# Kernel tuning notes

Hardware: AMD Instinct MI355X
Metric: run time of the kernel (lower is better)

The kernel has to match this reference:

```python
import jax, jax.numpy as jnp
import numpy as np

B, N = 32, 512
NB_TAU, NB_G, NB_W = 8, 8, 6
FLOOR = 0.001
SLOPE_RANGE = (0.5, 4.0)
BIAS_RANGE = (-2.0, 2.0)


def _basis(x, nb, kind):
    # MonotoneBasis: fixed grid of slopes/biases, monotone activation per basis.
    slopes = jnp.asarray(np.linspace(SLOPE_RANGE[0], SLOPE_RANGE[1], nb), x.dtype)
    biases = jnp.asarray(np.linspace(BIAS_RANGE[0], BIAS_RANGE[1], nb), x.dtype)
    z = x[..., None] * slopes + biases  # [..., nb]
    return jax.nn.softplus(z) if kind == 'softplus' else jax.nn.sigmoid(z)


def _normalize_scores(scores, mask, eps=1e-6):
    scores = jnp.where(mask, scores, 0.0)
    denom = jnp.clip(mask.sum(axis=1, keepdims=True), 1)
    mean = scores.sum(axis=1, keepdims=True) / denom
    scores = scores - mean
    var = (scores ** 2 * mask).sum(axis=1, keepdims=True) / denom
    return scores / jnp.sqrt(var + eps)


def setup_inputs() -> dict:
    key = jax.random.key(0)
    k1, k2, k3, k4, k5 = jax.random.split(key, 5)
    return {
        'predictions': jax.random.normal(k1, (B, N), dtype=jnp.float32),
        # targets in [0,1): all valid (no -1 padding), ties have measure zero
        'targets': jax.random.uniform(k2, (B, N), dtype=jnp.float32),
        'theta_tau': jax.random.normal(k3, (NB_TAU,), dtype=jnp.float32) * 0.1,
        'theta_g': jax.random.normal(k4, (NB_G,), dtype=jnp.float32) * 0.1,
        'theta_w': jax.random.normal(k5, (NB_W,), dtype=jnp.float32) * 0.1,
    }


def reference(predictions, targets, theta_tau, theta_g, theta_w):
    mask = ~jnp.isclose(targets, -1.0)
    s = _normalize_scores(predictions, mask)
    r = targets
    n = predictions.shape[1]
    iu, ju = np.triu_indices(n, k=1)  # static pair enumeration, P = n*(n-1)/2

    dr = r[:, iu] - r[:, ju]                      # [B, P]
    t = jnp.sign(dr)
    keep = (t != 0) & mask[:, iu] & mask[:, ju]   # drop ties / padded pairs
    ds = s[:, iu] - s[:, ju]
    abs_dr = jnp.abs(dr)

    # learned nonnegative combination coefficients (monotone outputs)
    c_tau = jax.nn.softplus(theta_tau)
    c_g = jax.nn.softplus(theta_g)
    c_w = jax.nn.softplus(theta_w)

    tau = _basis(abs_dr, NB_TAU, 'softplus') @ c_tau   # learned margin
    m = tau - t * ds
    g = _basis(m, NB_G, 'softplus') @ c_g              # learned penalty
    w = FLOOR + _basis(abs_dr, NB_W, 'sigmoid') @ c_w  # learned gap weight
    pair_loss = g * w

    kf = keep.astype(pair_loss.dtype)
    denom = jnp.clip(kf.sum(axis=1), 1.0)
    row_loss = (pair_loss * kf).sum(axis=1) / denom    # per-row mean over kept pairs
    valid_row = (kf.sum(axis=1) > 0).astype(pair_loss.dtype)
    return (row_loss * valid_row).sum() / jnp.clip(valid_row.sum(), 1.0)
```

## Files before the change

kernel.cpp:

```cpp
#include <hip/hip_runtime.h>
#include <math.h>

#define BB 32
#define NN 512

#define OFF_RS2 0
#define OFF_CF  32768
#define OFF_SUM 32808
#define OFF_CNT 32840

__device__ __forceinline__ float splus(float z) {
    return fmaxf(z, 0.0f) + __logf(1.0f + __expf(-fabsf(z)));
}

__device__ __constant__ float ST8[8] = {0.5f, 1.0f, 1.5f, 2.0f, 2.5f, 3.0f, 3.5f, 4.0f};
__device__ __constant__ float BT8[8] = {
    (float)(-2.0), (float)(-2.0 + 4.0/7.0), (float)(-2.0 + 8.0/7.0),
    (float)(-2.0 + 12.0/7.0), (float)(-2.0 + 16.0/7.0),
    (float)(-2.0 + 20.0/7.0), (float)(-2.0 + 24.0/7.0), 2.0f };
__device__ __constant__ float SW6[6] = {0.5f, (float)(0.5 + 3.5/5.0), (float)(0.5 + 7.0/5.0),
    (float)(0.5 + 10.5/5.0), (float)(0.5 + 14.0/5.0), 4.0f};
__device__ __constant__ float BW6[6] = {-2.0f, (float)(-2.0 + 4.0/5.0), (float)(-2.0 + 8.0/5.0),
    (float)(-2.0 + 12.0/5.0), (float)(-2.0 + 16.0/5.0), 2.0f};

__device__ __constant__ float TC[10][10] = {
    {1,0,0,0,0,0,0,0,0,0},
    {0,1,0,0,0,0,0,0,0,0},
    {-1,0,2,0,0,0,0,0,0,0},
    {0,-3,0,4,0,0,0,0,0,0},
    {1,0,-8,0,8,0,0,0,0,0},
    {0,5,0,-20,0,16,0,0,0,0},
    {-1,0,18,0,-48,0,32,0,0,0},
    {0,-7,0,56,0,-112,0,64,0,0},
    {1,0,-32,0,160,0,-256,0,128,0},
    {0,9,0,-120,0,432,0,-576,0,256},
};

__global__ __launch_bounds__(256)
void prep_kernel(const float* __restrict__ pred, const float* __restrict__ targ,
                 const float* __restrict__ th_tau, const float* __restrict__ th_g,
                 const float* __restrict__ th_w, float* __restrict__ ws)
{
    const int bid = blockIdx.x, tid = threadIdx.x;
    if (bid < BB) {
        const int base = bid * NN;
        float x0 = pred[base + tid], x1 = pred[base + tid + 256];
        float t0 = targ[base + tid], t1 = targ[base + tid + 256];
        bool v0 = fabsf(t0 + 1.0f) > 1.00001e-5f;
        bool v1 = fabsf(t1 + 1.0f) > 1.00001e-5f;
        float m0 = v0 ? 1.0f : 0.0f, m1 = v1 ? 1.0f : 0.0f;
        float xs0 = x0 * m0, xs1 = x1 * m1;
        float lsum = xs0 + xs1;
        float lsq  = xs0 * xs0 + xs1 * xs1;
        float lcnt = m0 + m1;
        #pragma unroll
        for (int off = 32; off; off >>= 1) {
            lsum += __shfl_down(lsum, off);
            lsq  += __shfl_down(lsq,  off);
            lcnt += __shfl_down(lcnt, off);
        }
        __shared__ float red[3][4];
        const int lane = tid & 63, wv = tid >> 6;
        if (lane == 0) { red[0][wv] = lsum; red[1][wv] = lsq; red[2][wv] = lcnt; }
        __syncthreads();
        __shared__ float mean_s, rsig_s;
        if (tid == 0) {
            float S = 0.0f, Q = 0.0f, C = 0.0f;
            for (int i = 0; i < 4; i++) { S += red[0][i]; Q += red[1][i]; C += red[2][i]; }
            float denom = fmaxf(C, 1.0f);
            float mean = S / denom;
            float var = Q / denom - mean * mean;
            mean_s = mean;
            rsig_s = 1.0f / sqrtf(var + 1e-6f);
            ws[OFF_SUM + bid] = 0.0f;
            ws[OFF_CNT + bid] = 0.0f;
        }
        __syncthreads();
        const float qnan = __uint_as_float(0x7fc00000u);
        float2* RS2 = (float2*)(ws + OFF_RS2);
        RS2[base + tid]       = make_float2(v0 ? t0 : qnan, (xs0 - mean_s) * rsig_s);
        RS2[base + tid + 256] = make_float2(v1 ? t1 : qnan, (xs1 - mean_s) * rsig_s);
    } else {
        const int wv = tid >> 6, lane = tid & 63;
        __shared__ float fbuf[4][64];
        __shared__ float cbuf[4][10];
        float u = __cosf((float)M_PI * ((float)lane + 0.5f) * (1.0f / 64.0f));
        float f;
        if (wv == 0) {
            float xv = fmaf(0.5f, u, 0.5f);
            f = 0.0f;
            #pragma unroll
            for (int k = 0; k < 8; k++)
                f = fmaf(splus(fmaf(xv, ST8[k], BT8[k])), splus(th_tau[k]), f);
        } else if (wv == 1) {
            float xv = fmaf(0.5f, u, 0.5f);
            f = 0.001f;
            #pragma unroll
            for (int k = 0; k < 6; k++) {
                float z = fmaf(xv, SW6[k], BW6[k]);
                f = fmaf(1.0f / (1.0f + __expf(-z)), splus(th_w[k]), f);
            }
        } else {
            float xv = fmaf(8.0f, u, 8.0f);
            float gp = 0.0f, gn = 0.0f;
            #pragma unroll
            for (int k = 0; k < 8; k++) {
                float c = splus(th_g[k]);
                gp = fmaf(splus(fmaf( xv, ST8[k], BT8[k])), c, gp);
                gn = fmaf(splus(fmaf(-xv, ST8[k], BT8[k])), c, gn);
            }
            f = (wv == 2) ? 0.5f * (gp + gn) : 0.5f * (gp - gn);
        }
        fbuf[wv][lane] = f;
        __syncthreads();
        const int nc   = (wv < 2) ? 6 : 10;
        const int base = (wv == 0) ? 0 : (wv == 1) ? 6 : (wv == 2) ? 12 : 22;
        if (lane < nc) {
            float c = 0.0f;
            for (int i = 0; i < 64; i++)
                c += fbuf[wv][i] * __cosf((float)M_PI * (float)lane * ((float)i + 0.5f) * (1.0f / 64.0f));
            c *= (lane == 0) ? (1.0f / 64.0f) : (2.0f / 64.0f);
            cbuf[wv][lane] = c;
        }
        __syncthreads();
        if (lane < nc) {
            float mono = 0.0f;
            for (int j = 0; j < nc; j++) mono += cbuf[wv][j] * TC[j][lane];
            ws[OFF_CF + base + lane] = mono;
        }
        if (wv == 2 && lane == 0) {
            float gB = 0.0f;
            #pragma unroll
            for (int k = 0; k < 8; k++) gB += splus(th_g[k]) * ST8[k];
            ws[OFF_CF + 32] = gB;
        }
    }
}

__global__ __launch_bounds__(256)
void pair_kernel(const float2* __restrict__ RS2, const float* __restrict__ CF,
                 float* __restrict__ sums)
{
    const int b   = blockIdx.x & (BB - 1);
    const int sub = blockIdx.x >> 5;
    const int tid = threadIdx.x;
    __shared__ float2 sRS[768];
    sRS[tid]       = RS2[b * NN + tid];
    sRS[tid + 256] = RS2[b * NN + tid + 256];
    sRS[tid + 512] = RS2[b * NN + tid];

    float ct[6], cw[6], ce[10], co[10];
    #pragma unroll
    for (int k = 0; k < 6; k++)  ct[k] = CF[k];
    #pragma unroll
    for (int k = 0; k < 6; k++)  cw[k] = CF[6 + k];
    #pragma unroll
    for (int k = 0; k < 10; k++) ce[k] = CF[12 + k];
    #pragma unroll
    for (int k = 0; k < 10; k++) co[k] = CF[22 + k];
    const float gB = CF[32];
    __syncthreads();

    float lsum = 0.0f, lcnt = 0.0f;

    auto do_pair = [&](float2 a, float2 q, bool allow) {
        float dr  = a.x - q.x;
        float ds  = a.y - q.y;
        unsigned sgn = __float_as_uint(dr) & 0x80000000u;
        float tds = __uint_as_float(__float_as_uint(ds) ^ sgn);
        float t1  = fmaf(fabsf(dr), 2.0f, -1.0f);
        float tau = fmaf(ct[5], t1, ct[4]);
        tau = fmaf(tau, t1, ct[3]); tau = fmaf(tau, t1, ct[2]);
        tau = fmaf(tau, t1, ct[1]); tau = fmaf(tau, t1, ct[0]);
        float w = fmaf(cw[5], t1, cw[4]);
        w = fmaf(w, t1, cw[3]); w = fmaf(w, t1, cw[2]);
        w = fmaf(w, t1, cw[1]); w = fmaf(w, t1, cw[0]);
        float m  = tau - tds;
        float au = fminf(fabsf(m), 16.0f);
        float tg = fmaf(au, 0.125f, -1.0f);
        float E = ce[9], O = co[9];
        #pragma unroll
        for (int k = 8; k >= 0; k--) {
            E = fmaf(E, tg, ce[k]);
            O = fmaf(O, tg, co[k]);
        }
        unsigned msgn = __float_as_uint(m) & 0x80000000u;
        float g = E + __uint_as_float(__float_as_uint(O) ^ msgn);
        g = fmaf(fmaxf(m - 16.0f, 0.0f), gB, g);
        float p = g * w;
        bool keep = __builtin_islessgreater(dr, 0.0f) && allow;
        lsum = keep ? (lsum + p) : lsum;
        lcnt = keep ? (lcnt + 1.0f) : lcnt;
    };

    const int d0 = sub * 8 + 1;
    const float2 a0 = sRS[tid];
    const float2 a1 = sRS[tid + 256];
    const float2* pj0 = &sRS[tid + d0];
    const float2* pj1 = &sRS[tid + 256 + d0];
    const bool lastsub = (sub == 31);
    #pragma unroll
    for (int k = 0; k < 8; k++)
        do_pair(a0, pj0[k], true);
    #pragma unroll
    for (int k = 0; k < 7; k++)
        do_pair(a1, pj1[k], true);
    do_pair(a1, pj1[7], !lastsub);

    #pragma unroll
    for (int off = 32; off; off >>= 1) {
        lsum += __shfl_down(lsum, off);
        lcnt += __shfl_down(lcnt, off);
    }
    __shared__ float red[2][4];
    const int lane = tid & 63, wv = tid >> 6;
    if (lane == 0) { red[0][wv] = lsum; red[1][wv] = lcnt; }
    __syncthreads();
    if (tid == 0) {
        float S = red[0][0] + red[0][1] + red[0][2] + red[0][3];
        float C = red[1][0] + red[1][1] + red[1][2] + red[1][3];
        atomicAdd(sums + b, S);
        atomicAdd(sums + BB + b, C);
    }
}

__global__ void final_kernel(const float* __restrict__ sums, float* __restrict__ out)
{
    const int tid = threadIdx.x;
    float val = 0.0f, vld = 0.0f;
    if (tid < BB) {
        float s = sums[tid], c = sums[BB + tid];
        float rl = s / fmaxf(c, 1.0f);
        float v  = (c > 0.0f) ? 1.0f : 0.0f;
        val = rl * v;
        vld = v;
    }
    #pragma unroll
    for (int off = 32; off; off >>= 1) {
        val += __shfl_down(val, off);
        vld += __shfl_down(vld, off);
    }
    if (tid == 0) out[0] = val / fmaxf(vld, 1.0f);
}

extern "C" void kernel_launch(void* const* d_in, const int* in_sizes, int n_in,
                              void* d_out, int out_size, void* d_ws, size_t ws_size,
                              hipStream_t stream) {
    const float* pred   = (const float*)d_in[0];
    const float* targ   = (const float*)d_in[1];
    const float* th_tau = (const float*)d_in[2];
    const float* th_g   = (const float*)d_in[3];
    const float* th_w   = (const float*)d_in[4];
    float* ws  = (float*)d_ws;
    float* out = (float*)d_out;

    prep_kernel<<<BB + 1, 256, 0, stream>>>(pred, targ, th_tau, th_g, th_w, ws);
    pair_kernel<<<BB * 32, 256, 0, stream>>>((const float2*)(ws + OFF_RS2),
                                             ws + OFF_CF, ws + OFF_SUM);
    final_kernel<<<1, 64, 0, stream>>>(ws + OFF_SUM, out);
}
```

Measured before the change: 76.74 us.

## Fuse prep and pair kernels, recompute stats and coefficients per block

Merges the prep and pair kernels into one kernel where every block recomputes its row's mean/variance and the Chebyshev coefficients in shared memory. This removes a kernel launch and the global round-trip for the normalized scores. Blocks per row drop from 32 to 16, so each block handles twice as many diagonals. Global atomics are replaced by per-block partials that a 512-thread final kernel reduces. The cost is redundant coefficient work in every block (cosine sums over 64 points) and half as many blocks.

```diff
diff --git a/kernel.cpp b/kernel.cpp
--- a/kernel.cpp
+++ b/kernel.cpp
@@ -3,11 +3,7 @@
 
 #define BB 32
 #define NN 512
-
-#define OFF_RS2 0
-#define OFF_CF  32768
-#define OFF_SUM 32808
-#define OFF_CNT 32840
+#define NSUB 16
 
 __device__ __forceinline__ float splus(float z) {
     return fmaxf(z, 0.0f) + __logf(1.0f + __expf(-fabsf(z)));
@@ -37,53 +33,41 @@
 };
 
 __global__ __launch_bounds__(256)
-void prep_kernel(const float* __restrict__ pred, const float* __restrict__ targ,
-                 const float* __restrict__ th_tau, const float* __restrict__ th_g,
-                 const float* __restrict__ th_w, float* __restrict__ ws)
+void fused_kernel(const float* __restrict__ pred, const float* __restrict__ targ,
+                  const float* __restrict__ th_tau, const float* __restrict__ th_g,
+                  const float* __restrict__ th_w, float2* __restrict__ part)
 {
-    const int bid = blockIdx.x, tid = threadIdx.x;
-    if (bid < BB) {
-        const int base = bid * NN;
-        float x0 = pred[base + tid], x1 = pred[base + tid + 256];
-        float t0 = targ[base + tid], t1 = targ[base + tid + 256];
-        bool v0 = fabsf(t0 + 1.0f) > 1.00001e-5f;
-        bool v1 = fabsf(t1 + 1.0f) > 1.00001e-5f;
-        float m0 = v0 ? 1.0f : 0.0f, m1 = v1 ? 1.0f : 0.0f;
-        float xs0 = x0 * m0, xs1 = x1 * m1;
+    const int b   = blockIdx.x & (BB - 1);
+    const int sub = blockIdx.x >> 5;
+    const int tid = threadIdx.x;
+    const int lane = tid & 63, wv = tid >> 6;
+
+    __shared__ float2 sRS[768];
+    __shared__ float  red[3][4];
+    __shared__ float  fbuf[4][64];
+    __shared__ float  cbuf[4][10];
+    __shared__ float  cf[40];
+    __shared__ float  mean_s, rsig_s;
+
+    const int base = b * NN;
+    float x0 = pred[base + tid], x1 = pred[base + tid + 256];
+    float t0 = targ[base + tid], t1 = targ[base + tid + 256];
+    bool v0 = fabsf(t0 + 1.0f) > 1.00001e-5f;
+    bool v1 = fabsf(t1 + 1.0f) > 1.00001e-5f;
+    float xs0 = v0 ? x0 : 0.0f, xs1 = v1 ? x1 : 0.0f;
+    {
         float lsum = xs0 + xs1;
         float lsq  = xs0 * xs0 + xs1 * xs1;
-        float lcnt = m0 + m1;
+        float lcnt = (v0 ? 1.0f : 0.0f) + (v1 ? 1.0f : 0.0f);
         #pragma unroll
         for (int off = 32; off; off >>= 1) {
             lsum += __shfl_down(lsum, off);
             lsq  += __shfl_down(lsq,  off);
             lcnt += __shfl_down(lcnt, off);
         }
-        __shared__ float red[3][4];
-        const int lane = tid & 63, wv = tid >> 6;
         if (lane == 0) { red[0][wv] = lsum; red[1][wv] = lsq; red[2][wv] = lcnt; }
-        __syncthreads();
-        __shared__ float mean_s, rsig_s;
-        if (tid == 0) {
-            float S = 0.0f, Q = 0.0f, C = 0.0f;
-            for (int i = 0; i < 4; i++) { S += red[0][i]; Q += red[1][i]; C += red[2][i]; }
-            float denom = fmaxf(C, 1.0f);
-            float mean = S / denom;
-            float var = Q / denom - mean * mean;
-            mean_s = mean;
-            rsig_s = 1.0f / sqrtf(var + 1e-6f);
-            ws[OFF_SUM + bid] = 0.0f;
-            ws[OFF_CNT + bid] = 0.0f;
-        }
-        __syncthreads();
-        const float qnan = __uint_as_float(0x7fc00000u);
-        float2* RS2 = (float2*)(ws + OFF_RS2);
-        RS2[base + tid]       = make_float2(v0 ? t0 : qnan, (xs0 - mean_s) * rsig_s);
-        RS2[base + tid + 256] = make_float2(v1 ? t1 : qnan, (xs1 - mean_s) * rsig_s);
-    } else {
-        const int wv = tid >> 6, lane = tid & 63;
-        __shared__ float fbuf[4][64];
-        __shared__ float cbuf[4][10];
+    }
+    {
         float u = __cosf((float)M_PI * ((float)lane + 0.5f) * (1.0f / 64.0f));
         float f;
         if (wv == 0) {
@@ -112,69 +96,69 @@
             f = (wv == 2) ? 0.5f * (gp + gn) : 0.5f * (gp - gn);
         }
         fbuf[wv][lane] = f;
-        __syncthreads();
-        const int nc   = (wv < 2) ? 6 : 10;
-        const int base = (wv == 0) ? 0 : (wv == 1) ? 6 : (wv == 2) ? 12 : 22;
+    }
+    __syncthreads();
+
+    if (tid == 0) {
+        float S = 0.0f, Q = 0.0f, C = 0.0f;
+        for (int i = 0; i < 4; i++) { S += red[0][i]; Q += red[1][i]; C += red[2][i]; }
+        float denom = fmaxf(C, 1.0f);
+        float mean = S / denom;
+        float var = Q / denom - mean * mean;
+        mean_s = mean;
+        rsig_s = 1.0f / sqrtf(var + 1e-6f);
+    }
+    {
+        const int nc    = (wv < 2) ? 6 : 10;
+        const int cbase = (wv == 0) ? 0 : (wv == 1) ? 6 : (wv == 2) ? 12 : 22;
         if (lane < nc) {
             float c = 0.0f;
             for (int i = 0; i < 64; i++)
                 c += fbuf[wv][i] * __cosf((float)M_PI * (float)lane * ((float)i + 0.5f) * (1.0f / 64.0f));
             c *= (lane == 0) ? (1.0f / 64.0f) : (2.0f / 64.0f);
             cbuf[wv][lane] = c;
-        }
-        __syncthreads();
-        if (lane < nc) {
             float mono = 0.0f;
             for (int j = 0; j < nc; j++) mono += cbuf[wv][j] * TC[j][lane];
-            ws[OFF_CF + base + lane] = mono;
+            cf[cbase + lane] = mono;
         }
         if (wv == 2 && lane == 0) {
             float gB = 0.0f;
             #pragma unroll
             for (int k = 0; k < 8; k++) gB += splus(th_g[k]) * ST8[k];
-            ws[OFF_CF + 32] = gB;
-        }
-    }
-}
-
-__global__ __launch_bounds__(256)
-void pair_kernel(const float2* __restrict__ RS2, const float* __restrict__ CF,
-                 float* __restrict__ sums)
-{
-    const int b   = blockIdx.x & (BB - 1);
-    const int sub = blockIdx.x >> 5;
-    const int tid = threadIdx.x;
-    __shared__ float2 sRS[768];
-    sRS[tid]       = RS2[b * NN + tid];
-    sRS[tid + 256] = RS2[b * NN + tid + 256];
-    sRS[tid + 512] = RS2[b * NN + tid];
-
+            cf[32] = gB;
+        }
+    }
+    __syncthreads();
+
+    const float qnan = __uint_as_float(0x7fc00000u);
+    float2 e0 = make_float2(v0 ? t0 : qnan, (xs0 - mean_s) * rsig_s);
+    float2 e1 = make_float2(v1 ? t1 : qnan, (xs1 - mean_s) * rsig_s);
+    sRS[tid] = e0; sRS[tid + 256] = e1; sRS[tid + 512] = e0;
     float ct[6], cw[6], ce[10], co[10];
     #pragma unroll
-    for (int k = 0; k < 6; k++)  ct[k] = CF[k];
-    #pragma unroll
-    for (int k = 0; k < 6; k++)  cw[k] = CF[6 + k];
-    #pragma unroll
-    for (int k = 0; k < 10; k++) ce[k] = CF[12 + k];
-    #pragma unroll
-    for (int k = 0; k < 10; k++) co[k] = CF[22 + k];
-    const float gB = CF[32];
+    for (int k = 0; k < 6; k++)  ct[k] = cf[k];
+    #pragma unroll
+    for (int k = 0; k < 6; k++)  cw[k] = cf[6 + k];
+    #pragma unroll
+    for (int k = 0; k < 10; k++) ce[k] = cf[12 + k];
+    #pragma unroll
+    for (int k = 0; k < 10; k++) co[k] = cf[22 + k];
+    const float gB = cf[32];
     __syncthreads();
 
     float lsum = 0.0f, lcnt = 0.0f;
-
     auto do_pair = [&](float2 a, float2 q, bool allow) {
         float dr  = a.x - q.x;
         float ds  = a.y - q.y;
         unsigned sgn = __float_as_uint(dr) & 0x80000000u;
         float tds = __uint_as_float(__float_as_uint(ds) ^ sgn);
-        float t1  = fmaf(fabsf(dr), 2.0f, -1.0f);
-        float tau = fmaf(ct[5], t1, ct[4]);
-        tau = fmaf(tau, t1, ct[3]); tau = fmaf(tau, t1, ct[2]);
-        tau = fmaf(tau, t1, ct[1]); tau = fmaf(tau, t1, ct[0]);
-        float w = fmaf(cw[5], t1, cw[4]);
-        w = fmaf(w, t1, cw[3]); w = fmaf(w, t1, cw[2]);
-        w = fmaf(w, t1, cw[1]); w = fmaf(w, t1, cw[0]);
+        float t1v = fmaf(fabsf(dr), 2.0f, -1.0f);
+        float tau = fmaf(ct[5], t1v, ct[4]);
+        tau = fmaf(tau, t1v, ct[3]); tau = fmaf(tau, t1v, ct[2]);
+        tau = fmaf(tau, t1v, ct[1]); tau = fmaf(tau, t1v, ct[0]);
+        float w = fmaf(cw[5], t1v, cw[4]);
+        w = fmaf(w, t1v, cw[3]); w = fmaf(w, t1v, cw[2]);
+        w = fmaf(w, t1v, cw[1]); w = fmaf(w, t1v, cw[0]);
         float m  = tau - tds;
         float au = fminf(fabsf(m), 16.0f);
         float tg = fmaf(au, 0.125f, -1.0f);
@@ -193,54 +177,58 @@
         lcnt = keep ? (lcnt + 1.0f) : lcnt;
     };
 
-    const int d0 = sub * 8 + 1;
+    const int d0 = sub * 16 + 1;
     const float2 a0 = sRS[tid];
     const float2 a1 = sRS[tid + 256];
-    const float2* pj0 = &sRS[tid + d0];
-    const float2* pj1 = &sRS[tid + 256 + d0];
-    const bool lastsub = (sub == 31);
-    #pragma unroll
-    for (int k = 0; k < 8; k++)
-        do_pair(a0, pj0[k], true);
-    #pragma unroll
-    for (int k = 0; k < 7; k++)
-        do_pair(a1, pj1[k], true);
-    do_pair(a1, pj1[7], !lastsub);
+    const float2* p0 = &sRS[tid + d0];
+    const float2* p1 = &sRS[tid + 256 + d0];
+    #pragma unroll
+    for (int k = 0; k < 16; k++) do_pair(a0, p0[k], true);
+    #pragma unroll
+    for (int k = 0; k < 15; k++) do_pair(a1, p1[k], true);
+    do_pair(a1, p1[15], sub != NSUB - 1);
 
     #pragma unroll
     for (int off = 32; off; off >>= 1) {
         lsum += __shfl_down(lsum, off);
         lcnt += __shfl_down(lcnt, off);
     }
-    __shared__ float red[2][4];
-    const int lane = tid & 63, wv = tid >> 6;
     if (lane == 0) { red[0][wv] = lsum; red[1][wv] = lcnt; }
     __syncthreads();
     if (tid == 0) {
         float S = red[0][0] + red[0][1] + red[0][2] + red[0][3];
         float C = red[1][0] + red[1][1] + red[1][2] + red[1][3];
-        atomicAdd(sums + b, S);
-        atomicAdd(sums + BB + b, C);
-    }
-}
-
-__global__ void final_kernel(const float* __restrict__ sums, float* __restrict__ out)
+        part[blockIdx.x] = make_float2(S, C);
+    }
+}
+
+__global__ __launch_bounds__(512)
+void final_kernel(const float2* __restrict__ part, float* __restrict__ out)
 {
     const int tid = threadIdx.x;
-    float val = 0.0f, vld = 0.0f;
-    if (tid < BB) {
-        float s = sums[tid], c = sums[BB + tid];
-        float rl = s / fmaxf(c, 1.0f);
-        float v  = (c > 0.0f) ? 1.0f : 0.0f;
-        val = rl * v;
-        vld = v;
-    }
-    #pragma unroll
-    for (int off = 32; off; off >>= 1) {
-        val += __shfl_down(val, off);
-        vld += __shfl_down(vld, off);
-    }
-    if (tid == 0) out[0] = val / fmaxf(vld, 1.0f);
+    __shared__ float rs[BB], rc[BB];
+    if (tid < BB) { rs[tid] = 0.0f; rc[tid] = 0.0f; }
+    __syncthreads();
+    float2 p = part[tid];
+    atomicAdd(&rs[tid & (BB - 1)], p.x);
+    atomicAdd(&rc[tid & (BB - 1)], p.y);
+    __syncthreads();
+    if (tid < 64) {
+        float val = 0.0f, vld = 0.0f;
+        if (tid < BB) {
+            float c = rc[tid], s = rs[tid];
+            float rl = s / fmaxf(c, 1.0f);
+            float v  = (c > 0.0f) ? 1.0f : 0.0f;
+            val = rl * v;
+            vld = v;
+        }
+        #pragma unroll
+        for (int off = 32; off; off >>= 1) {
+            val += __shfl_down(val, off);
+            vld += __shfl_down(vld, off);
+        }
+        if (tid == 0) out[0] = val / fmaxf(vld, 1.0f);
+    }
 }
 
 extern "C" void kernel_launch(void* const* d_in, const int* in_sizes, int n_in,
@@ -251,11 +239,9 @@
     const float* th_tau = (const float*)d_in[2];
     const float* th_g   = (const float*)d_in[3];
     const float* th_w   = (const float*)d_in[4];
-    float* ws  = (float*)d_ws;
-    float* out = (float*)d_out;
-
-    prep_kernel<<<BB + 1, 256, 0, stream>>>(pred, targ, th_tau, th_g, th_w, ws);
-    pair_kernel<<<BB * 32, 256, 0, stream>>>((const float2*)(ws + OFF_RS2),
-                                             ws + OFF_CF, ws + OFF_SUM);
-    final_kernel<<<1, 64, 0, stream>>>(ws + OFF_SUM, out);
-}
+    float2* part = (float2*)d_ws;
+    float* out   = (float*)d_out;
+
+    fused_kernel<<<BB * NSUB, 256, 0, stream>>>(pred, targ, th_tau, th_g, th_w, part);
+    final_kernel<<<1, 512, 0, stream>>>(part, out);
+}
```

Result: faster. 72.87 us (-5.0%).
